# Optimization experiments

Hardware: AMD Instinct MI355X
Metric: run time of the kernel (lower is better)

The kernel has to match this reference:

```python
import jax, jax.numpy as jnp
import numpy as np

HIDDEN = 2048
NUM_HEADS = 16
HEAD_DIM = 128
KV_C = 512
Q_C = 1536
ROPE_DIM = 64
B, S = 2, 2048


def _rope(x):
    # x: [B, H, S, D] with D even; interleaved-pair rotation as in the torch module
    b, h, s, d = x.shape
    inv_freq = 1.0 / (10000.0 ** (jnp.arange(0, d, 2, dtype=jnp.float32) / d))  # [d/2]
    pos = jnp.arange(s, dtype=jnp.float32)
    sinusoid = pos[:, None] * inv_freq[None, :]  # [S, d/2]
    sin, cos = jnp.sin(sinusoid), jnp.cos(sinusoid)
    xr = x.reshape(b, h, s, d // 2, 2)
    x1, x2 = xr[..., 0], xr[..., 1]
    out = jnp.stack([x1 * cos - x2 * sin, x1 * sin + x2 * cos], axis=-1)
    return out.reshape(b, h, s, d)


def setup_inputs() -> dict:
    key = jax.random.key(0)
    ks = jax.random.split(key, 12)

    def lin(k, fan_in, fan_out):
        k1, k2 = jax.random.split(k)
        lim = 1.0 / np.sqrt(fan_in)
        w = jax.random.uniform(k1, (fan_in, fan_out), jnp.float32, -lim, lim)
        b = jax.random.uniform(k2, (fan_out,), jnp.float32, -lim, lim)
        return w, b

    kv_down_w, kv_down_b = lin(ks[0], HIDDEN, KV_C)
    key_up_w, key_up_b = lin(ks[1], KV_C, NUM_HEADS * HEAD_DIM)
    value_up_w, value_up_b = lin(ks[2], KV_C, NUM_HEADS * HEAD_DIM)
    key_rope_w, key_rope_b = lin(ks[3], KV_C, NUM_HEADS * ROPE_DIM)
    query_down_w, query_down_b = lin(ks[4], HIDDEN, Q_C)
    query_up_w, query_up_b = lin(ks[5], Q_C, NUM_HEADS * HEAD_DIM)
    query_rope_w, query_rope_b = lin(ks[6], Q_C, NUM_HEADS * ROPE_DIM)
    out_w, out_b = lin(ks[7], NUM_HEADS * HEAD_DIM, HIDDEN)

    x = jax.random.normal(ks[8], (B, S, HIDDEN), jnp.float32)
    attention_mask = jnp.ones((B, S), dtype=jnp.bool_)  # all tokens valid

    return dict(x=x, attention_mask=attention_mask,
                kv_down_w=kv_down_w, kv_down_b=kv_down_b,
                key_up_w=key_up_w, key_up_b=key_up_b,
                value_up_w=value_up_w, value_up_b=value_up_b,
                key_rope_w=key_rope_w, key_rope_b=key_rope_b,
                query_down_w=query_down_w, query_down_b=query_down_b,
                query_up_w=query_up_w, query_up_b=query_up_b,
                query_rope_w=query_rope_w, query_rope_b=query_rope_b,
                out_w=out_w, out_b=out_b)


def reference(x, attention_mask,
              kv_down_w, kv_down_b, key_up_w, key_up_b,
              value_up_w, value_up_b, key_rope_w, key_rope_b,
              query_down_w, query_down_b, query_up_w, query_up_b,
              query_rope_w, query_rope_b, out_w, out_b):
    b, s, _ = x.shape

    kv_c = x @ kv_down_w + kv_down_b                                 # [B,S,KV_C]
    keys_c = (kv_c @ key_up_w + key_up_b).reshape(b, s, NUM_HEADS, HEAD_DIM).transpose(0, 2, 1, 3)
    values = (kv_c @ value_up_w + value_up_b).reshape(b, s, NUM_HEADS, HEAD_DIM).transpose(0, 2, 1, 3)
    keys_r = (kv_c @ key_rope_w + key_rope_b).reshape(b, s, NUM_HEADS, ROPE_DIM).transpose(0, 2, 1, 3)
    keys_r = _rope(keys_r)

    q_c = x @ query_down_w + query_down_b                            # [B,S,Q_C]
    queries_c = (q_c @ query_up_w + query_up_b).reshape(b, s, NUM_HEADS, HEAD_DIM).transpose(0, 2, 1, 3)
    queries_r = (q_c @ query_rope_w + query_rope_b).reshape(b, s, NUM_HEADS, ROPE_DIM).transpose(0, 2, 1, 3)
    queries_r = _rope(queries_r)

    queries = jnp.concatenate([queries_c, queries_r], axis=-1)      # [B,H,S,HD+RD]
    keys = jnp.concatenate([keys_c, keys_r], axis=-1)

    scale = 1.0 / np.sqrt(HEAD_DIM + ROPE_DIM)
    scores = jnp.einsum('bhqd,bhkd->bhqk', queries, keys) * scale   # [B,H,S,S]

    causal = jnp.triu(jnp.ones((s, s), dtype=jnp.bool_), k=1)       # True = masked
    pad = ~attention_mask                                            # [B,S], True = masked key
    mask = causal[None, None, :, :] | pad[:, None, None, :]
    scores = jnp.where(mask, jnp.float32(-1e9), scores)

    probs = jax.nn.softmax(scores, axis=-1)
    context = jnp.einsum('bhqk,bhkd->bhqd', probs, values)          # [B,H,S,HD]
    context = context.transpose(0, 2, 1, 3).reshape(b, s, NUM_HEADS * HEAD_DIM)
    return context @ out_w + out_b                                   # [B,S,HIDDEN]
```

## Files before the change

kernel.cpp:

```cpp
#include <hip/hip_runtime.h>

typedef unsigned short u16;
typedef short short8 __attribute__((ext_vector_type(8)));
typedef short short4v __attribute__((ext_vector_type(4)));
typedef float floatx4 __attribute__((ext_vector_type(4)));
typedef float floatx4v __attribute__((ext_vector_type(4)));

#define SQ 2048
#define NH 16
#define HD 128
#define RD 64
#define NB 2
#define LDKV 5120
#define LDQ 3072

#define LKC 136
#define LKR 72
#define LVT 72
#define LP  72

__device__ __forceinline__ float bf2f(u16 u) {
  union { unsigned u; float f; } v; v.u = ((unsigned)u) << 16; return v.f;
}
__device__ __forceinline__ u16 f2bf(float f) {
  union { float f; unsigned u; } v; v.f = f;
  return (u16)((v.u + 0x7FFFu + ((v.u >> 16) & 1u)) >> 16);
}
__device__ __forceinline__ void gll16(const u16* g, u16* l) {
  __builtin_amdgcn_global_load_lds((const __attribute__((address_space(1))) void*)g,
                                   (__attribute__((address_space(3))) void*)l, 16, 0, 0);
}

__global__ __launch_bounds__(256) void convert_x(const float* __restrict__ src,
                                                 u16* __restrict__ dst, int n4) {
  const int i = blockIdx.x * 256 + threadIdx.x;
  if (i >= n4) return;
  const floatx4v v = *(const floatx4v*)(src + 4 * (size_t)i);
  short4v o;
  o.x = (short)f2bf(v.x); o.y = (short)f2bf(v.y);
  o.z = (short)f2bf(v.z); o.w = (short)f2bf(v.w);
  *(short4v*)(dst + 4 * (size_t)i) = o;
}

__global__ __launch_bounds__(256) void convert_biases(
    const float* b0, const float* b1, const float* b2, const float* b3,
    const float* b4, const float* b5, const float* b6, const float* b7,
    u16* __restrict__ bc) {
  const int i = blockIdx.x * 256 + threadIdx.x;
  if (i >= 12288) return;
  float v;
  if      (i < 512)   v = b0[i];
  else if (i < 2048)  v = b1[i - 512];
  else if (i < 4096)  v = b2[i - 2048];
  else if (i < 6144)  v = b3[i - 4096];
  else if (i < 7168)  v = b4[i - 6144];
  else if (i < 9216)  v = b5[i - 7168];
  else if (i < 10240) v = b6[i - 9216];
  else                v = b7[i - 10240];
  bc[i] = f2bf(v);
}

__global__ __launch_bounds__(256) void transpose_w(const float* __restrict__ in,
                                                   u16* __restrict__ out,
                                                   int R, int C) {
  __shared__ u16 tile[32][33];
  const int c0 = blockIdx.x * 32, r0 = blockIdx.y * 32;
  const int x = threadIdx.x & 31, y = threadIdx.x >> 5;
#pragma unroll
  for (int i = 0; i < 32; i += 8)
    tile[y + i][x] = f2bf(in[(size_t)(r0 + y + i) * C + c0 + x]);
  __syncthreads();
#pragma unroll
  for (int i = 0; i < 32; i += 8)
    out[(size_t)(c0 + y + i) * R + r0 + x] = tile[x][y + i];
}

__global__ __launch_bounds__(256) void transpose_v(const u16* __restrict__ KV,
                                                   u16* __restrict__ Vt) {
  __shared__ u16 tile[32][33];
  const int bh = blockIdx.z, b = bh >> 4, hh = bh & 15;
  const u16* pin = KV + (size_t)b * SQ * LDKV + 2048 + (size_t)hh * HD;
  u16* pout = Vt + (size_t)bh * HD * SQ;
  const int s0 = blockIdx.x * 32, d0 = blockIdx.y * 32;
  const int x = threadIdx.x & 31, y = threadIdx.x >> 5;
#pragma unroll
  for (int i = 0; i < 32; i += 8)
    tile[y + i][x] = pin[(size_t)(s0 + y + i) * LDKV + d0 + x];
  __syncthreads();
#pragma unroll
  for (int i = 0; i < 32; i += 8)
    pout[(size_t)(d0 + y + i) * SQ + s0 + x] = tile[x][y + i];
}

__global__ __launch_bounds__(256) void rope_inplace(u16* __restrict__ buf,
                                                    int ld, int coloff) {
  const int i = blockIdx.x * 256 + threadIdx.x;
  if (i >= NB * SQ * NH * 32) return;
  const int j = i & 31;
  const int hh = (i >> 5) & 15;
  const int row = i >> 9;
  const int s = row & (SQ - 1);
  u16* p = buf + (size_t)row * ld + coloff + hh * RD + 2 * j;
  const float x1 = bf2f(p[0]), x2 = bf2f(p[1]);
  const float inv = exp2f(-(float)j * 0.41524101186092031f);
  const float ang = (float)s * inv;
  float sn, cs;
  sincosf(ang, &sn, &cs);
  p[0] = f2bf(x1 * cs - x2 * sn);
  p[1] = f2bf(x1 * sn + x2 * cs);
}

__global__ __launch_bounds__(256) void gemm_bt(const u16* __restrict__ A, int lda,
                                               const u16* __restrict__ Bt,
                                               const u16* __restrict__ bias,
                                               void* __restrict__ Cout, int ldc,
                                               int wf32, int N, int K) {
  __shared__ __align__(16) u16 lA[128 * 32];
  __shared__ __align__(16) u16 lB[128 * 32];
  const int t = threadIdx.x;
  const int lane = t & 63, w = t >> 6;
  const int wm = w & 1, wn = w >> 1;
  const int m0 = blockIdx.y * 128, n0 = blockIdx.x * 128;
  const int srow = t >> 2, scol = (t & 3) * 8;
  const u16* gA = A + (size_t)(m0 + srow) * lda + scol;
  const u16* gB = Bt + (size_t)(n0 + srow) * K + scol;
  u16* lA0 = lA + (16 * w) * 32;
  u16* lA1 = lA + (64 + 16 * w) * 32;
  u16* lB0 = lB + (16 * w) * 32;
  u16* lB1 = lB + (64 + 16 * w) * 32;
  const int lane_m = lane & 15, lane_k = (lane >> 4) * 8;
  floatx4 acc[4][4] = {};
  for (int k0 = 0; k0 < K; k0 += 32) {
    gll16(gA + k0, lA0);
    gll16(gA + (size_t)64 * lda + k0, lA1);
    gll16(gB + k0, lB0);
    gll16(gB + (size_t)64 * K + k0, lB1);
    __syncthreads();
    short8 af[4], bf[4];
#pragma unroll
    for (int i = 0; i < 4; i++)
      af[i] = *(const short8*)(lA + (wm * 64 + i * 16 + lane_m) * 32 + lane_k);
#pragma unroll
    for (int i = 0; i < 4; i++)
      bf[i] = *(const short8*)(lB + (wn * 64 + i * 16 + lane_m) * 32 + lane_k);
#pragma unroll
    for (int mi = 0; mi < 4; mi++)
#pragma unroll
      for (int ni = 0; ni < 4; ni++)
        acc[mi][ni] = __builtin_amdgcn_mfma_f32_16x16x32_bf16(af[mi], bf[ni], acc[mi][ni], 0, 0, 0);
    __syncthreads();
  }
  const int quad = lane >> 4;
#pragma unroll
  for (int ni = 0; ni < 4; ni++) {
    const int col = n0 + wn * 64 + ni * 16 + lane_m;
    const float bv = bf2f(bias[col]);
#pragma unroll
    for (int mi = 0; mi < 4; mi++) {
      const int row = m0 + wm * 64 + mi * 16 + quad * 4;
      if (wf32) {
        float* pc = (float*)Cout + (size_t)row * ldc + col;
#pragma unroll
        for (int r = 0; r < 4; r++)
          pc[(size_t)r * ldc] = acc[mi][ni][r] + bv;
      } else {
        u16* pc = (u16*)Cout + (size_t)row * ldc + col;
#pragma unroll
        for (int r = 0; r < 4; r++)
          pc[(size_t)r * ldc] = f2bf(acc[mi][ni][r] + bv);
      }
    }
  }
}

__global__ __launch_bounds__(512, 4) void flash_attn(const u16* __restrict__ Q,
                                                     const u16* __restrict__ KV,
                                                     const u16* __restrict__ Vt,
                                                     u16* __restrict__ Ctx) {
  __shared__ __align__(16) u16 lKc[64 * LKC];
  __shared__ __align__(16) u16 lKr[64 * LKR];
  __shared__ __align__(16) u16 lVt[128 * LVT];
  __shared__ __align__(16) u16 lP[8 * 16 * LP];
  const int t = threadIdx.x, lane = t & 63, w = t >> 6;
  const int col = blockIdx.y;
  const int qtile = (col < 16) ? (15 - (int)blockIdx.x) : (int)blockIdx.x;
  const int h = col & (NH - 1);
  const int b = col >> 4;
  const int q0 = qtile * 128;
  const int nkt = 2 * qtile + 2;
  const int lane_m = lane & 15, quad = lane >> 4, lane_k = quad * 8;

  const int qrow = q0 + 16 * w + lane_m;
  const u16* qcp = Q + (size_t)(b * SQ + qrow) * LDQ + h * HD;
  const u16* qrp = Q + (size_t)(b * SQ + qrow) * LDQ + 2048 + h * RD;
  short8 qfc[4], qfr[2];
#pragma unroll
  for (int ks = 0; ks < 4; ks++) qfc[ks] = *(const short8*)(qcp + ks * 32 + lane_k);
#pragma unroll
  for (int ks = 0; ks < 2; ks++) qfr[ks] = *(const short8*)(qrp + ks * 32 + lane_k);

  floatx4 O[8] = {};
  float mrow[4], lsum[4];
#pragma unroll
  for (int r = 0; r < 4; r++) { mrow[r] = -1e30f; lsum[r] = 0.f; }

  const u16* gKc = KV + (size_t)b * SQ * LDKV + h * HD;
  const u16* gKr = KV + (size_t)b * SQ * LDKV + 4096 + h * RD;
  const u16* gVt = Vt + (size_t)(b * NH + h) * HD * SQ;
  const float C2 = 0.10412825525540364f;

  short8 rKc[2], rKr, rVt[2];
  auto load_tile = [&](int kb) {
#pragma unroll
    for (int i = 0; i < 2; i++) {
      const int c = t + i * 512, row = c >> 4, cc = (c & 15) * 8;
      rKc[i] = *(const short8*)(gKc + (size_t)(kb + row) * LDKV + cc);
    }
    {
      const int row = t >> 3, cc = (t & 7) * 8;
      rKr = *(const short8*)(gKr + (size_t)(kb + row) * LDKV + cc);
    }
#pragma unroll
    for (int i = 0; i < 2; i++) {
      const int c = t + i * 512, row = c >> 3, cc = (c & 7) * 8;
      rVt[i] = *(const short8*)(gVt + (size_t)row * SQ + kb + cc);
    }
  };

  const int wrow_lo = q0 + 16 * w;
  const int wrow_hi = wrow_lo + 15;

  load_tile(0);
  for (int kt = 0; kt < nkt; kt++) {
    const int kb = kt * 64;
    __syncthreads();
#pragma unroll
    for (int i = 0; i < 2; i++) {
      const int c = t + i * 512, row = c >> 4, cc = (c & 15) * 8;
      *(short8*)(lKc + row * LKC + cc) = rKc[i];
    }
    {
      const int row = t >> 3, cc = (t & 7) * 8;
      *(short8*)(lKr + row * LKR + cc) = rKr;
    }
#pragma unroll
    for (int i = 0; i < 2; i++) {
      const int c = t + i * 512, row = c >> 3, cc = (c & 7) * 8;
      *(short8*)(lVt + row * LVT + cc) = rVt[i];
    }
    __syncthreads();
    if (kt < nkt - 1) load_tile(kb + 64);

    if (kb <= wrow_hi) {
      float ss[4][4];
#pragma unroll
      for (int n = 0; n < 4; n++) {
        floatx4 a = {0.f, 0.f, 0.f, 0.f};
#pragma unroll
        for (int ks = 0; ks < 4; ks++) {
          const short8 kf = *(const short8*)(lKc + (n * 16 + lane_m) * LKC + ks * 32 + lane_k);
          a = __builtin_amdgcn_mfma_f32_16x16x32_bf16(qfc[ks], kf, a, 0, 0, 0);
        }
#pragma unroll
        for (int ks = 0; ks < 2; ks++) {
          const short8 kf = *(const short8*)(lKr + (n * 16 + lane_m) * LKR + ks * 32 + lane_k);
          a = __builtin_amdgcn_mfma_f32_16x16x32_bf16(qfr[ks], kf, a, 0, 0, 0);
        }
#pragma unroll
        for (int r = 0; r < 4; r++) ss[n][r] = a[r];
      }
      if (kb + 63 > wrow_lo) {
#pragma unroll
        for (int n = 0; n < 4; n++) {
          const int kcol = kb + n * 16 + lane_m;
#pragma unroll
          for (int r = 0; r < 4; r++) {
            const int row = wrow_lo + quad * 4 + r;
            if (kcol > row) ss[n][r] = -1e30f;
          }
        }
      }
      float pw[4][4];
#pragma unroll
      for (int r = 0; r < 4; r++) {
        float m = fmaxf(fmaxf(ss[0][r], ss[1][r]), fmaxf(ss[2][r], ss[3][r]));
#pragma unroll
        for (int d = 1; d < 16; d <<= 1) m = fmaxf(m, __shfl_xor(m, d));
        const float mn = fmaxf(mrow[r], m);
        const float alpha = exp2f((mrow[r] - mn) * C2);
        mrow[r] = mn;
        float s = 0.f;
#pragma unroll
        for (int n = 0; n < 4; n++) {
          const float p = exp2f((ss[n][r] - mn) * C2);
          pw[n][r] = p;
          s += p;
        }
#pragma unroll
        for (int d = 1; d < 16; d <<= 1) s += __shfl_xor(s, d);
        lsum[r] = lsum[r] * alpha + s;
#pragma unroll
        for (int vb = 0; vb < 8; vb++) O[vb][r] *= alpha;
      }
#pragma unroll
      for (int n = 0; n < 4; n++)
#pragma unroll
        for (int r = 0; r < 4; r++)
          lP[(w * 16 + quad * 4 + r) * LP + n * 16 + lane_m] = f2bf(pw[n][r]);
      asm volatile("s_waitcnt lgkmcnt(0)" ::: "memory");
#pragma unroll
      for (int ks = 0; ks < 2; ks++) {
        const short8 pf = *(const short8*)(lP + (w * 16 + lane_m) * LP + ks * 32 + lane_k);
#pragma unroll
        for (int vb = 0; vb < 8; vb++) {
          const short8 vf = *(const short8*)(lVt + (vb * 16 + lane_m) * LVT + ks * 32 + lane_k);
          O[vb] = __builtin_amdgcn_mfma_f32_16x16x32_bf16(pf, vf, O[vb], 0, 0, 0);
        }
      }
    }
  }
  float inv[4];
#pragma unroll
  for (int r = 0; r < 4; r++) inv[r] = 1.f / lsum[r];
#pragma unroll
  for (int vb = 0; vb < 8; vb++) {
#pragma unroll
    for (int r = 0; r < 4; r++) {
      const int row = wrow_lo + quad * 4 + r;
      Ctx[(size_t)(b * SQ + row) * 2048 + h * HD + vb * 16 + lane_m] = f2bf(O[vb][r] * inv[r]);
    }
  }
}

extern "C" void kernel_launch(void* const* d_in, const int* in_sizes, int n_in,
                              void* d_out, int out_size, void* d_ws, size_t ws_size,
                              hipStream_t stream) {
  (void)in_sizes; (void)n_in; (void)out_size; (void)ws_size;
  const float* x    = (const float*)d_in[0];
  const float* kvdw = (const float*)d_in[2];
  const float* kvdb = (const float*)d_in[3];
  const float* kuw  = (const float*)d_in[4];
  const float* kub  = (const float*)d_in[5];
  const float* vuw  = (const float*)d_in[6];
  const float* vub  = (const float*)d_in[7];
  const float* krw  = (const float*)d_in[8];
  const float* krb  = (const float*)d_in[9];
  const float* qdw  = (const float*)d_in[10];
  const float* qdb  = (const float*)d_in[11];
  const float* quw  = (const float*)d_in[12];
  const float* qub  = (const float*)d_in[13];
  const float* qrw  = (const float*)d_in[14];
  const float* qrb  = (const float*)d_in[15];
  const float* ow   = (const float*)d_in[16];
  const float* ob   = (const float*)d_in[17];

  u16* p = (u16*)d_ws;
  u16* bc   = p;  p += 16384;
  u16* WT1  = p;  p += (size_t)2048 * 2048;
  u16* WT2  = p;  p += (size_t)5120 * 512;
  u16* WT3  = p;  p += (size_t)3072 * 1536;
  u16* Ctx  = WT1;
  u16* WTo  = p;  p += (size_t)2048 * 2048;
  u16* KVQd = p;  p += (size_t)4096 * 2048;
  u16* Vt   = KVQd;
  u16* KV   = p;  p += (size_t)4096 * 5120;
  u16* Qb   = p;  p += (size_t)4096 * 3072;
  u16* xc   = Qb;

  convert_x<<<dim3(8192), 256, 0, stream>>>(x, xc, 4096 * 2048 / 4);
  convert_biases<<<dim3(48), 256, 0, stream>>>(kvdb, qdb, kub, vub, krb, qub, qrb, ob, bc);

  auto T = [&](const float* in, u16* out, int R, int C) {
    transpose_w<<<dim3(C / 32, R / 32), 256, 0, stream>>>(in, out, R, C);
  };
  T(kvdw, WT1, 2048, 512);
  T(qdw,  WT1 + (size_t)512 * 2048, 2048, 1536);
  T(kuw,  WT2, 512, 2048);
  T(vuw,  WT2 + (size_t)2048 * 512, 512, 2048);
  T(krw,  WT2 + (size_t)4096 * 512, 512, 1024);
  T(quw,  WT3, 1536, 2048);
  T(qrw,  WT3 + (size_t)2048 * 1536, 1536, 1024);
  T(ow,   WTo, 2048, 2048);

  auto G = [&](const u16* A, int lda, const u16* Bt, const u16* bias,
               void* Cout, int ldc, int wf32, int N, int K) {
    gemm_bt<<<dim3(N / 128, 4096 / 128), 256, 0, stream>>>(A, lda, Bt, bias, Cout, ldc, wf32, N, K);
  };
  G(xc, 2048, WT1, bc, KVQd, 2048, 0, 2048, 2048);
  G(KVQd, 2048, WT2, bc + 2048, KV, LDKV, 0, 5120, 512);
  G(KVQd + 512, 2048, WT3, bc + 7168, Qb, LDQ, 0, 3072, 1536);

  rope_inplace<<<dim3((NB * SQ * NH * 32) / 256), 256, 0, stream>>>(KV, LDKV, 4096);
  rope_inplace<<<dim3((NB * SQ * NH * 32) / 256), 256, 0, stream>>>(Qb, LDQ, 2048);
  transpose_v<<<dim3(SQ / 32, HD / 32, NB * NH), 256, 0, stream>>>(KV, Vt);
  flash_attn<<<dim3(16, 32), 512, 0, stream>>>(Qb, KV, Vt, Ctx);

  G(Ctx, 2048, WTo, bc + 10240, d_out, 2048, 1, 2048, 2048);
}
```

Measured before the change: 556.3 us.

## Unroll GEMM K-loop by two and double-buffer attention KV register prefetch

The GEMM now loads two 32-wide K slices into separate LDS buffers per iteration. That halves the number of barrier pairs and puts more global-to-LDS loads in flight. The attention kernel keeps two register sets of K/V tiles, so each tile is prefetched two steps ahead instead of one, which should hide more global load latency. In exchange, the attention kernel uses more VGPRs, which may reduce occupancy. The attention loop also assumes an even tile count per block, and the GEMM assumes K is a multiple of 64.

```diff
diff --git a/kernel.cpp b/kernel.cpp
--- a/kernel.cpp
+++ b/kernel.cpp
@@ -115,8 +115,10 @@
                                                const u16* __restrict__ bias,
                                                void* __restrict__ Cout, int ldc,
                                                int wf32, int N, int K) {
-  __shared__ __align__(16) u16 lA[128 * 32];
-  __shared__ __align__(16) u16 lB[128 * 32];
+  __shared__ __align__(16) u16 lAk0[128 * 32];
+  __shared__ __align__(16) u16 lAk1[128 * 32];
+  __shared__ __align__(16) u16 lBk0[128 * 32];
+  __shared__ __align__(16) u16 lBk1[128 * 32];
   const int t = threadIdx.x;
   const int lane = t & 63, w = t >> 6;
   const int wm = w & 1, wn = w >> 1;
@@ -124,30 +126,54 @@
   const int srow = t >> 2, scol = (t & 3) * 8;
   const u16* gA = A + (size_t)(m0 + srow) * lda + scol;
   const u16* gB = Bt + (size_t)(n0 + srow) * K + scol;
-  u16* lA0 = lA + (16 * w) * 32;
-  u16* lA1 = lA + (64 + 16 * w) * 32;
-  u16* lB0 = lB + (16 * w) * 32;
-  u16* lB1 = lB + (64 + 16 * w) * 32;
+  u16* lA00 = lAk0 + (16 * w) * 32;
+  u16* lA01 = lAk0 + (64 + 16 * w) * 32;
+  u16* lA10 = lAk1 + (16 * w) * 32;
+  u16* lA11 = lAk1 + (64 + 16 * w) * 32;
+  u16* lB00 = lBk0 + (16 * w) * 32;
+  u16* lB01 = lBk0 + (64 + 16 * w) * 32;
+  u16* lB10 = lBk1 + (16 * w) * 32;
+  u16* lB11 = lBk1 + (64 + 16 * w) * 32;
   const int lane_m = lane & 15, lane_k = (lane >> 4) * 8;
   floatx4 acc[4][4] = {};
-  for (int k0 = 0; k0 < K; k0 += 32) {
-    gll16(gA + k0, lA0);
-    gll16(gA + (size_t)64 * lda + k0, lA1);
-    gll16(gB + k0, lB0);
-    gll16(gB + (size_t)64 * K + k0, lB1);
-    __syncthreads();
-    short8 af[4], bf[4];
-#pragma unroll
-    for (int i = 0; i < 4; i++)
-      af[i] = *(const short8*)(lA + (wm * 64 + i * 16 + lane_m) * 32 + lane_k);
-#pragma unroll
-    for (int i = 0; i < 4; i++)
-      bf[i] = *(const short8*)(lB + (wn * 64 + i * 16 + lane_m) * 32 + lane_k);
-#pragma unroll
-    for (int mi = 0; mi < 4; mi++)
-#pragma unroll
-      for (int ni = 0; ni < 4; ni++)
-        acc[mi][ni] = __builtin_amdgcn_mfma_f32_16x16x32_bf16(af[mi], bf[ni], acc[mi][ni], 0, 0, 0);
+  for (int k0 = 0; k0 < K; k0 += 64) {
+    gll16(gA + k0, lA00);
+    gll16(gA + (size_t)64 * lda + k0, lA01);
+    gll16(gA + k0 + 32, lA10);
+    gll16(gA + (size_t)64 * lda + k0 + 32, lA11);
+    gll16(gB + k0, lB00);
+    gll16(gB + (size_t)64 * K + k0, lB01);
+    gll16(gB + k0 + 32, lB10);
+    gll16(gB + (size_t)64 * K + k0 + 32, lB11);
+    __syncthreads();
+    {
+      short8 af[4], bf[4];
+#pragma unroll
+      for (int i = 0; i < 4; i++)
+        af[i] = *(const short8*)(lAk0 + (wm * 64 + i * 16 + lane_m) * 32 + lane_k);
+#pragma unroll
+      for (int i = 0; i < 4; i++)
+        bf[i] = *(const short8*)(lBk0 + (wn * 64 + i * 16 + lane_m) * 32 + lane_k);
+#pragma unroll
+      for (int mi = 0; mi < 4; mi++)
+#pragma unroll
+        for (int ni = 0; ni < 4; ni++)
+          acc[mi][ni] = __builtin_amdgcn_mfma_f32_16x16x32_bf16(af[mi], bf[ni], acc[mi][ni], 0, 0, 0);
+    }
+    {
+      short8 af[4], bf[4];
+#pragma unroll
+      for (int i = 0; i < 4; i++)
+        af[i] = *(const short8*)(lAk1 + (wm * 64 + i * 16 + lane_m) * 32 + lane_k);
+#pragma unroll
+      for (int i = 0; i < 4; i++)
+        bf[i] = *(const short8*)(lBk1 + (wn * 64 + i * 16 + lane_m) * 32 + lane_k);
+#pragma unroll
+      for (int mi = 0; mi < 4; mi++)
+#pragma unroll
+        for (int ni = 0; ni < 4; ni++)
+          acc[mi][ni] = __builtin_amdgcn_mfma_f32_16x16x32_bf16(af[mi], bf[ni], acc[mi][ni], 0, 0, 0);
+    }
     __syncthreads();
   }
   const int quad = lane >> 4;
@@ -209,116 +235,130 @@
   const u16* gVt = Vt + (size_t)(b * NH + h) * HD * SQ;
   const float C2 = 0.10412825525540364f;
 
-  short8 rKc[2], rKr, rVt[2];
-  auto load_tile = [&](int kb) {
+  const int wrow_lo = q0 + 16 * w;
+  const int wrow_hi = wrow_lo + 15;
+
+  short8 rKc0[2], rKr0, rVt0[2];
+  short8 rKc1[2], rKr1, rVt1[2];
+
+  auto load_tile = [&](int kb, short8 (&Kc)[2], short8& Kr, short8 (&Vv)[2]) {
 #pragma unroll
     for (int i = 0; i < 2; i++) {
       const int c = t + i * 512, row = c >> 4, cc = (c & 15) * 8;
-      rKc[i] = *(const short8*)(gKc + (size_t)(kb + row) * LDKV + cc);
+      Kc[i] = *(const short8*)(gKc + (size_t)(kb + row) * LDKV + cc);
     }
     {
       const int row = t >> 3, cc = (t & 7) * 8;
-      rKr = *(const short8*)(gKr + (size_t)(kb + row) * LDKV + cc);
+      Kr = *(const short8*)(gKr + (size_t)(kb + row) * LDKV + cc);
     }
 #pragma unroll
     for (int i = 0; i < 2; i++) {
       const int c = t + i * 512, row = c >> 3, cc = (c & 7) * 8;
-      rVt[i] = *(const short8*)(gVt + (size_t)row * SQ + kb + cc);
+      Vv[i] = *(const short8*)(gVt + (size_t)row * SQ + kb + cc);
     }
   };
 
-  const int wrow_lo = q0 + 16 * w;
-  const int wrow_hi = wrow_lo + 15;
-
-  load_tile(0);
-  for (int kt = 0; kt < nkt; kt++) {
-    const int kb = kt * 64;
-    __syncthreads();
+  auto stage_lds = [&](short8 (&Kc)[2], short8& Kr, short8 (&Vv)[2]) {
 #pragma unroll
     for (int i = 0; i < 2; i++) {
       const int c = t + i * 512, row = c >> 4, cc = (c & 15) * 8;
-      *(short8*)(lKc + row * LKC + cc) = rKc[i];
+      *(short8*)(lKc + row * LKC + cc) = Kc[i];
     }
     {
       const int row = t >> 3, cc = (t & 7) * 8;
-      *(short8*)(lKr + row * LKR + cc) = rKr;
+      *(short8*)(lKr + row * LKR + cc) = Kr;
     }
 #pragma unroll
     for (int i = 0; i < 2; i++) {
       const int c = t + i * 512, row = c >> 3, cc = (c & 7) * 8;
-      *(short8*)(lVt + row * LVT + cc) = rVt[i];
-    }
-    __syncthreads();
-    if (kt < nkt - 1) load_tile(kb + 64);
-
-    if (kb <= wrow_hi) {
-      float ss[4][4];
+      *(short8*)(lVt + row * LVT + cc) = Vv[i];
+    }
+  };
+
+  auto compute = [&](int kb) {
+    float ss[4][4];
+#pragma unroll
+    for (int n = 0; n < 4; n++) {
+      floatx4 a = {0.f, 0.f, 0.f, 0.f};
+#pragma unroll
+      for (int ks = 0; ks < 4; ks++) {
+        const short8 kf = *(const short8*)(lKc + (n * 16 + lane_m) * LKC + ks * 32 + lane_k);
+        a = __builtin_amdgcn_mfma_f32_16x16x32_bf16(qfc[ks], kf, a, 0, 0, 0);
+      }
+#pragma unroll
+      for (int ks = 0; ks < 2; ks++) {
+        const short8 kf = *(const short8*)(lKr + (n * 16 + lane_m) * LKR + ks * 32 + lane_k);
+        a = __builtin_amdgcn_mfma_f32_16x16x32_bf16(qfr[ks], kf, a, 0, 0, 0);
+      }
+#pragma unroll
+      for (int r = 0; r < 4; r++) ss[n][r] = a[r];
+    }
+    if (kb + 63 > wrow_lo) {
 #pragma unroll
       for (int n = 0; n < 4; n++) {
-        floatx4 a = {0.f, 0.f, 0.f, 0.f};
-#pragma unroll
-        for (int ks = 0; ks < 4; ks++) {
-          const short8 kf = *(const short8*)(lKc + (n * 16 + lane_m) * LKC + ks * 32 + lane_k);
-          a = __builtin_amdgcn_mfma_f32_16x16x32_bf16(qfc[ks], kf, a, 0, 0, 0);
+        const int kcol = kb + n * 16 + lane_m;
+#pragma unroll
+        for (int r = 0; r < 4; r++) {
+          const int row = wrow_lo + quad * 4 + r;
+          if (kcol > row) ss[n][r] = -1e30f;
         }
-#pragma unroll
-        for (int ks = 0; ks < 2; ks++) {
-          const short8 kf = *(const short8*)(lKr + (n * 16 + lane_m) * LKR + ks * 32 + lane_k);
-          a = __builtin_amdgcn_mfma_f32_16x16x32_bf16(qfr[ks], kf, a, 0, 0, 0);
-        }
-#pragma unroll
-        for (int r = 0; r < 4; r++) ss[n][r] = a[r];
-      }
-      if (kb + 63 > wrow_lo) {
-#pragma unroll
-        for (int n = 0; n < 4; n++) {
-          const int kcol = kb + n * 16 + lane_m;
-#pragma unroll
-          for (int r = 0; r < 4; r++) {
-            const int row = wrow_lo + quad * 4 + r;
-            if (kcol > row) ss[n][r] = -1e30f;
-          }
-        }
-      }
-      float pw[4][4];
-#pragma unroll
-      for (int r = 0; r < 4; r++) {
-        float m = fmaxf(fmaxf(ss[0][r], ss[1][r]), fmaxf(ss[2][r], ss[3][r]));
-#pragma unroll
-        for (int d = 1; d < 16; d <<= 1) m = fmaxf(m, __shfl_xor(m, d));
-        const float mn = fmaxf(mrow[r], m);
-        const float alpha = exp2f((mrow[r] - mn) * C2);
-        mrow[r] = mn;
-        float s = 0.f;
-#pragma unroll
-        for (int n = 0; n < 4; n++) {
-          const float p = exp2f((ss[n][r] - mn) * C2);
-          pw[n][r] = p;
-          s += p;
-        }
-#pragma unroll
-        for (int d = 1; d < 16; d <<= 1) s += __shfl_xor(s, d);
-        lsum[r] = lsum[r] * alpha + s;
-#pragma unroll
-        for (int vb = 0; vb < 8; vb++) O[vb][r] *= alpha;
-      }
-#pragma unroll
-      for (int n = 0; n < 4; n++)
-#pragma unroll
-        for (int r = 0; r < 4; r++)
-          lP[(w * 16 + quad * 4 + r) * LP + n * 16 + lane_m] = f2bf(pw[n][r]);
-      asm volatile("s_waitcnt lgkmcnt(0)" ::: "memory");
-#pragma unroll
-      for (int ks = 0; ks < 2; ks++) {
-        const short8 pf = *(const short8*)(lP + (w * 16 + lane_m) * LP + ks * 32 + lane_k);
-#pragma unroll
-        for (int vb = 0; vb < 8; vb++) {
-          const short8 vf = *(const short8*)(lVt + (vb * 16 + lane_m) * LVT + ks * 32 + lane_k);
-          O[vb] = __builtin_amdgcn_mfma_f32_16x16x32_bf16(pf, vf, O[vb], 0, 0, 0);
-        }
-      }
-    }
+      }
+    }
+    float pw[4][4];
+#pragma unroll
+    for (int r = 0; r < 4; r++) {
+      float m = fmaxf(fmaxf(ss[0][r], ss[1][r]), fmaxf(ss[2][r], ss[3][r]));
+#pragma unroll
+      for (int d = 1; d < 16; d <<= 1) m = fmaxf(m, __shfl_xor(m, d));
+      const float mn = fmaxf(mrow[r], m);
+      const float alpha = exp2f((mrow[r] - mn) * C2);
+      mrow[r] = mn;
+      float s = 0.f;
+#pragma unroll
+      for (int n = 0; n < 4; n++) {
+        const float p = exp2f((ss[n][r] - mn) * C2);
+        pw[n][r] = p;
+        s += p;
+      }
+#pragma unroll
+      for (int d = 1; d < 16; d <<= 1) s += __shfl_xor(s, d);
+      lsum[r] = lsum[r] * alpha + s;
+#pragma unroll
+      for (int vb = 0; vb < 8; vb++) O[vb][r] *= alpha;
+    }
+#pragma unroll
+    for (int n = 0; n < 4; n++)
+#pragma unroll
+      for (int r = 0; r < 4; r++)
+        lP[(w * 16 + quad * 4 + r) * LP + n * 16 + lane_m] = f2bf(pw[n][r]);
+    asm volatile("s_waitcnt lgkmcnt(0)" ::: "memory");
+#pragma unroll
+    for (int ks = 0; ks < 2; ks++) {
+      const short8 pf = *(const short8*)(lP + (w * 16 + lane_m) * LP + ks * 32 + lane_k);
+#pragma unroll
+      for (int vb = 0; vb < 8; vb++) {
+        const short8 vf = *(const short8*)(lVt + (vb * 16 + lane_m) * LVT + ks * 32 + lane_k);
+        O[vb] = __builtin_amdgcn_mfma_f32_16x16x32_bf16(pf, vf, O[vb], 0, 0, 0);
+      }
+    }
+  };
+
+  load_tile(0, rKc0, rKr0, rVt0);
+  load_tile(64, rKc1, rKr1, rVt1);
+  for (int kt = 0; kt < nkt; kt += 2) {
+    const int kb0 = kt * 64, kb1 = kb0 + 64;
+    __syncthreads();
+    stage_lds(rKc0, rKr0, rVt0);
+    __syncthreads();
+    if (kt + 2 < nkt) load_tile(kb0 + 128, rKc0, rKr0, rVt0);
+    if (kb0 <= wrow_hi) compute(kb0);
+    __syncthreads();
+    stage_lds(rKc1, rKr1, rVt1);
+    __syncthreads();
+    if (kt + 3 < nkt) load_tile(kb1 + 128, rKc1, rKr1, rVt1);
+    if (kb1 <= wrow_hi) compute(kb1);
   }
+
   float inv[4];
 #pragma unroll
   for (int r = 0; r < 4; r++) inv[r] = 1.f / lsum[r];
```

Measured after the change: 619.7 us. +11.4%, slower.

## Double-buffer GEMM LDS, swizzle blocks across XCDs, lazy softmax rescale, MFMA priority

Applied to the files above, without the earlier changes.

The GEMM now double-buffers its LDS tiles. It issues the async global-to-LDS loads for the next K slice before computing the current one, which removes one barrier per iteration. Block IDs are also remapped so consecutive tiles land on the same XCD, for better L2 reuse. In the attention kernel, the running-max rescale of O and lsum only happens when some row's tile max exceeds the stored max by a threshold, which skips most alpha multiplies. The MFMA sections are wrapped in s_setprio. The lazy rescale lets unnormalized probabilities grow to about 8x before rebasing, and the swizzle assumes the workgroup count is divisible by 8.

```diff
diff --git a/kernel.cpp b/kernel.cpp
--- a/kernel.cpp
+++ b/kernel.cpp
@@ -115,40 +115,49 @@
                                                const u16* __restrict__ bias,
                                                void* __restrict__ Cout, int ldc,
                                                int wf32, int N, int K) {
-  __shared__ __align__(16) u16 lA[128 * 32];
-  __shared__ __align__(16) u16 lB[128 * 32];
+  __shared__ __align__(16) u16 lA[2][128 * 32];
+  __shared__ __align__(16) u16 lB[2][128 * 32];
   const int t = threadIdx.x;
   const int lane = t & 63, w = t >> 6;
   const int wm = w & 1, wn = w >> 1;
-  const int m0 = blockIdx.y * 128, n0 = blockIdx.x * 128;
+  const int gx = gridDim.x;
+  const int nwg = gx * gridDim.y;
+  const int bid = blockIdx.y * gx + blockIdx.x;
+  const int cpx = nwg >> 3;
+  const int sbid = (bid & 7) * cpx + (bid >> 3);
+  const int m0 = (sbid / gx) * 128, n0 = (sbid % gx) * 128;
   const int srow = t >> 2, scol = (t & 3) * 8;
   const u16* gA = A + (size_t)(m0 + srow) * lda + scol;
   const u16* gB = Bt + (size_t)(n0 + srow) * K + scol;
-  u16* lA0 = lA + (16 * w) * 32;
-  u16* lA1 = lA + (64 + 16 * w) * 32;
-  u16* lB0 = lB + (16 * w) * 32;
-  u16* lB1 = lB + (64 + 16 * w) * 32;
   const int lane_m = lane & 15, lane_k = (lane >> 4) * 8;
+
+  auto stage = [&](int b, int k0) {
+    gll16(gA + k0, lA[b] + (16 * w) * 32);
+    gll16(gA + (size_t)64 * lda + k0, lA[b] + (64 + 16 * w) * 32);
+    gll16(gB + k0, lB[b] + (16 * w) * 32);
+    gll16(gB + (size_t)64 * K + k0, lB[b] + (64 + 16 * w) * 32);
+  };
+
   floatx4 acc[4][4] = {};
+  stage(0, 0);
+  __syncthreads();
+  int cur = 0;
   for (int k0 = 0; k0 < K; k0 += 32) {
-    gll16(gA + k0, lA0);
-    gll16(gA + (size_t)64 * lda + k0, lA1);
-    gll16(gB + k0, lB0);
-    gll16(gB + (size_t)64 * K + k0, lB1);
-    __syncthreads();
+    if (k0 + 32 < K) stage(cur ^ 1, k0 + 32);
     short8 af[4], bf[4];
 #pragma unroll
     for (int i = 0; i < 4; i++)
-      af[i] = *(const short8*)(lA + (wm * 64 + i * 16 + lane_m) * 32 + lane_k);
+      af[i] = *(const short8*)(lA[cur] + (wm * 64 + i * 16 + lane_m) * 32 + lane_k);
 #pragma unroll
     for (int i = 0; i < 4; i++)
-      bf[i] = *(const short8*)(lB + (wn * 64 + i * 16 + lane_m) * 32 + lane_k);
+      bf[i] = *(const short8*)(lB[cur] + (wn * 64 + i * 16 + lane_m) * 32 + lane_k);
 #pragma unroll
     for (int mi = 0; mi < 4; mi++)
 #pragma unroll
       for (int ni = 0; ni < 4; ni++)
         acc[mi][ni] = __builtin_amdgcn_mfma_f32_16x16x32_bf16(af[mi], bf[ni], acc[mi][ni], 0, 0, 0);
     __syncthreads();
+    cur ^= 1;
   }
   const int quad = lane >> 4;
 #pragma unroll
@@ -208,6 +217,7 @@
   const u16* gKr = KV + (size_t)b * SQ * LDKV + 4096 + h * RD;
   const u16* gVt = Vt + (size_t)(b * NH + h) * HD * SQ;
   const float C2 = 0.10412825525540364f;
+  const float THR = 28.8f;
 
   short8 rKc[2], rKr, rVt[2];
   auto load_tile = [&](int kb) {
@@ -253,6 +263,7 @@
 
     if (kb <= wrow_hi) {
       float ss[4][4];
+      __builtin_amdgcn_s_setprio(1);
 #pragma unroll
       for (int n = 0; n < 4; n++) {
         floatx4 a = {0.f, 0.f, 0.f, 0.f};
@@ -269,6 +280,7 @@
 #pragma unroll
         for (int r = 0; r < 4; r++) ss[n][r] = a[r];
       }
+      __builtin_amdgcn_s_setprio(0);
       if (kb + 63 > wrow_lo) {
 #pragma unroll
         for (int n = 0; n < 4; n++) {
@@ -280,27 +292,40 @@
           }
         }
       }
-      float pw[4][4];
+      float mt[4];
 #pragma unroll
       for (int r = 0; r < 4; r++) {
         float m = fmaxf(fmaxf(ss[0][r], ss[1][r]), fmaxf(ss[2][r], ss[3][r]));
 #pragma unroll
         for (int d = 1; d < 16; d <<= 1) m = fmaxf(m, __shfl_xor(m, d));
-        const float mn = fmaxf(mrow[r], m);
-        const float alpha = exp2f((mrow[r] - mn) * C2);
-        mrow[r] = mn;
+        mt[r] = m;
+      }
+      const bool grow = (mt[0] > mrow[0] + THR) || (mt[1] > mrow[1] + THR) ||
+                        (mt[2] > mrow[2] + THR) || (mt[3] > mrow[3] + THR);
+      if (__any(grow)) {
+#pragma unroll
+        for (int r = 0; r < 4; r++) {
+          const float mn = fmaxf(mrow[r], mt[r]);
+          const float alpha = exp2f((mrow[r] - mn) * C2);
+          mrow[r] = mn;
+          lsum[r] *= alpha;
+#pragma unroll
+          for (int vb = 0; vb < 8; vb++) O[vb][r] *= alpha;
+        }
+      }
+      float pw[4][4];
+#pragma unroll
+      for (int r = 0; r < 4; r++) {
         float s = 0.f;
 #pragma unroll
         for (int n = 0; n < 4; n++) {
-          const float p = exp2f((ss[n][r] - mn) * C2);
+          const float p = exp2f((ss[n][r] - mrow[r]) * C2);
           pw[n][r] = p;
           s += p;
         }
 #pragma unroll
         for (int d = 1; d < 16; d <<= 1) s += __shfl_xor(s, d);
-        lsum[r] = lsum[r] * alpha + s;
-#pragma unroll
-        for (int vb = 0; vb < 8; vb++) O[vb][r] *= alpha;
+        lsum[r] += s;
       }
 #pragma unroll
       for (int n = 0; n < 4; n++)
@@ -308,6 +333,7 @@
         for (int r = 0; r < 4; r++)
           lP[(w * 16 + quad * 4 + r) * LP + n * 16 + lane_m] = f2bf(pw[n][r]);
       asm volatile("s_waitcnt lgkmcnt(0)" ::: "memory");
+      __builtin_amdgcn_s_setprio(1);
 #pragma unroll
       for (int ks = 0; ks < 2; ks++) {
         const short8 pf = *(const short8*)(lP + (w * 16 + lane_m) * LP + ks * 32 + lane_k);
@@ -317,6 +343,7 @@
           O[vb] = __builtin_amdgcn_mfma_f32_16x16x32_bf16(pf, vf, O[vb], 0, 0, 0);
         }
       }
+      __builtin_amdgcn_s_setprio(0);
     }
   }
   float inv[4];
```

New measurement: 536.0 us. 1.04x faster.
